# Performance work log

Measured on AMD Instinct MI355X. Metric: run time of the kernel, lower is better.

The kernel has to match this reference:

```python
import jax, jax.numpy as jnp
import numpy as np

N_NODES = 100000
N_EDGES = 800000
NUM_GRAPHS = 64


def _lin_init(key, fan_in, fan_out):
    k1, k2 = jax.random.split(key)
    s = 1.0 / np.sqrt(fan_in)
    W = jax.random.uniform(k1, (fan_in, fan_out), jnp.float32, -s, s)
    b = jax.random.uniform(k2, (fan_out,), jnp.float32, -s, s)
    return W, b


def setup_inputs() -> dict:
    key = jax.random.key(0)
    ks = jax.random.split(key, 20)
    inp = {
        'x1': jax.random.normal(ks[0], (N_NODES, 384), jnp.float32),
        'x2': jax.random.normal(ks[1], (N_NODES, 32), jnp.float32),
        'pe': jax.random.normal(ks[2], (N_NODES, 64), jnp.float32),
        'edge_index': jax.random.randint(ks[3], (2, N_EDGES), 0, N_NODES, jnp.int32),
        'batch': jnp.sort(jax.random.randint(ks[4], (N_NODES,), 0, NUM_GRAPHS, jnp.int32)),
    }
    # parameters (fan_in, fan_out) per __init__ dims
    inp['Wc'], inp['bc'] = _lin_init(ks[5], 384, 192)     # embed_contraction
    inp['Wmf'], inp['bmf'] = _lin_init(ks[6], 192, 256)   # mpnn_feature
    inp['Wgf'], inp['bgf'] = _lin_init(ks[7], 256, 192)   # gcn_feature
    inp['Wmc'], inp['bmc'] = _lin_init(ks[8], 32, 64)     # mpnn_class
    inp['Wgc'], inp['bgc'] = _lin_init(ks[9], 64, 192)    # gcn_class
    inp['Wa1'], inp['ba1'] = _lin_init(ks[10], 192, 256)  # attention_nn[0]
    inp['Wa2'], inp['ba2'] = _lin_init(ks[11], 256, 192)  # attention_nn[2]
    inp['Wgd'], inp['bgd'] = _lin_init(ks[12], 192, 192)  # gcn_decoder
    inp['Wd1'], inp['bd1'] = _lin_init(ks[13], 192, 192)  # mpnn_decoder1
    inp['Wd2'], inp['bd2'] = _lin_init(ks[14], 192, 192)  # mpnn_decoder2
    inp['Wd3'], inp['bd3'] = _lin_init(ks[15], 192, 384)  # mpnn_decoder3
    return inp


def _mpnn(x, src, dst, W, b):
    # aggr='add': scatter-add gathered source features to targets, then Linear
    agg = jax.ops.segment_sum(x[src], dst, num_segments=N_NODES)
    return agg @ W + b


def _gcn(x, src, dst, W, b):
    # GCNConv with default self-loops and symmetric deg^-1/2 normalization
    h = x @ W
    deg = jax.ops.segment_sum(jnp.ones(src.shape[0], h.dtype), dst, num_segments=N_NODES) + 1.0
    dinv = jax.lax.rsqrt(deg)
    norm = dinv[src] * dinv[dst]
    agg = jax.ops.segment_sum(h[src] * norm[:, None], dst, num_segments=N_NODES)
    agg = agg + h * (dinv * dinv)[:, None]  # self-loop contribution
    return agg + b


def reference(x1, x2, pe, edge_index, batch,
              Wc, bc, Wmf, bmf, Wgf, bgf, Wmc, bmc, Wgc, bgc,
              Wa1, ba1, Wa2, ba2, Wgd, bgd, Wd1, bd1, Wd2, bd2, Wd3, bd3):
    src, dst = edge_index[0], edge_index[1]
    pe3 = jnp.concatenate([pe, pe, pe], axis=-1)  # [N, 192]

    # ---- encoder ----
    x1_res = jax.nn.relu(x1 @ Wc + bc)            # [N, 192]
    h = x1_res + pe3
    h = jax.nn.relu(_mpnn(h, src, dst, Wmf, bmf))  # [N, 256]
    h = jax.nn.relu(_gcn(h, src, dst, Wgf, bgf))   # [N, 192]
    c = jax.nn.relu(_mpnn(x2, src, dst, Wmc, bmc)) # [N, 64]
    c = jax.nn.relu(_gcn(c, src, dst, Wgc, bgc))   # [N, 192]
    z = h + c + x1_res

    # attentional aggregation: gate = attention_nn(z), segment softmax, weighted sum
    gate = jax.nn.relu(z @ Wa1 + ba1) @ Wa2 + ba2   # [N, 192]
    gmax = jax.ops.segment_max(gate, batch, num_segments=NUM_GRAPHS)
    e = jnp.exp(gate - gmax[batch])
    esum = jax.ops.segment_sum(e, batch, num_segments=NUM_GRAPHS)
    alpha = e / esum[batch]
    zg = jax.ops.segment_sum(alpha * z, batch, num_segments=NUM_GRAPHS)  # [B, 192]

    # ---- decoder ----
    z1 = zg[batch]                                  # broadcast graph embedding to nodes
    z1_res = jax.nn.relu(_gcn(z1, src, dst, Wgd, bgd))
    t = z1_res + pe3
    t = jax.nn.relu(_mpnn(t, src, dst, Wd1, bd1))
    t = jax.nn.relu(_mpnn(t, src, dst, Wd2, bd2)) + z1_res
    out = jax.nn.relu(_mpnn(t, src, dst, Wd3, bd3))  # [N, 384]
    return out
```

## Files before the change

kernel.cpp:

```cpp
#include <hip/hip_runtime.h>
#include <math.h>

#define N_NODES 100000
#define N_EDGES 800000
#define NGRAPH  64

typedef __attribute__((ext_vector_type(8))) __bf16 bf16x8;
typedef __attribute__((ext_vector_type(4))) float f32x4;

static __device__ __forceinline__ unsigned flip_f(float x) {
  unsigned u = __float_as_uint(x);
  return u ^ ((u & 0x80000000u) ? 0xFFFFFFFFu : 0x80000000u);
}
static __device__ __forceinline__ float unflip_f(unsigned m) {
  unsigned u = m ^ ((m & 0x80000000u) ? 0x80000000u : 0xFFFFFFFFu);
  return __uint_as_float(u);
}
static __device__ __forceinline__ unsigned short f2bf(float x) {
  unsigned u = __float_as_uint(x);
  u += 0x7fffu + ((u >> 16) & 1u);
  return (unsigned short)(u >> 16);
}
static __device__ __forceinline__ unsigned pk2(float a, float b) {
  return (unsigned)f2bf(a) | ((unsigned)f2bf(b) << 16);
}
static __device__ __forceinline__ float bf2f(unsigned short h) {
  return __uint_as_float((unsigned)h << 16);
}
static __device__ __forceinline__ void unpack8(uint4 w, float* f) {
  f[0] = __uint_as_float(w.x << 16); f[1] = __uint_as_float(w.x & 0xFFFF0000u);
  f[2] = __uint_as_float(w.y << 16); f[3] = __uint_as_float(w.y & 0xFFFF0000u);
  f[4] = __uint_as_float(w.z << 16); f[5] = __uint_as_float(w.z & 0xFFFF0000u);
  f[6] = __uint_as_float(w.w << 16); f[7] = __uint_as_float(w.w & 0xFFFF0000u);
}
static __device__ __forceinline__ uint4 pack8(const float* f) {
  uint4 w;
  w.x = pk2(f[0], f[1]); w.y = pk2(f[2], f[3]);
  w.z = pk2(f[4], f[5]); w.w = pk2(f[6], f[7]);
  return w;
}

__global__ void hist_k(const int* __restrict__ dst, int* __restrict__ cnt) {
  int e = blockIdx.x * 256 + threadIdx.x;
  if (e < N_EDGES) atomicAdd(&cnt[dst[e]], 1);
}

__global__ void dinv_k(const int* __restrict__ cnt, float* __restrict__ dinv) {
  int i = blockIdx.x * 256 + threadIdx.x;
  if (i < N_NODES) dinv[i] = rsqrtf((float)cnt[i] + 1.0f);
}

__global__ void scan_block_k(const int* __restrict__ cnt, int* __restrict__ rs,
                             int* __restrict__ bsum) {
  __shared__ int s[256];
  int t = threadIdx.x, i = blockIdx.x * 256 + t;
  int v = (i < N_NODES) ? cnt[i] : 0;
  s[t] = v; __syncthreads();
  for (int off = 1; off < 256; off <<= 1) {
    int a = (t >= off) ? s[t - off] : 0;
    __syncthreads();
    s[t] += a;
    __syncthreads();
  }
  if (i < N_NODES) rs[i] = s[t] - v;
  if (t == 255) bsum[blockIdx.x] = s[255];
}

__global__ void scan_bsum_k(int* __restrict__ bsum, int nb) {
  __shared__ int s[512];
  int t = threadIdx.x;
  int v = (t < nb) ? bsum[t] : 0;
  s[t] = v; __syncthreads();
  for (int off = 1; off < 512; off <<= 1) {
    int a = (t >= off) ? s[t - off] : 0;
    __syncthreads();
    s[t] += a;
    __syncthreads();
  }
  if (t < nb) bsum[t] = s[t] - v;
}

__global__ void scan_add_k(int* __restrict__ rs, int* __restrict__ cursor,
                           const int* __restrict__ bsum) {
  int i = blockIdx.x * 256 + threadIdx.x;
  if (i < N_NODES) {
    int r = rs[i] + bsum[i >> 8];
    rs[i] = r;
    cursor[i] = r;
  }
}

__global__ void build_k(const int* __restrict__ src, const int* __restrict__ dst,
                        int* __restrict__ cursor, int* __restrict__ srcs) {
  int e = blockIdx.x * 256 + threadIdx.x;
  if (e < N_EDGES) {
    int d = dst[e];
    int p = atomicAdd(&cursor[d], 1);
    srcs[p] = src[e];
  }
}

__global__ void graph_starts_k(const int* __restrict__ batch, int* __restrict__ gstart) {
  int g = threadIdx.x;
  if (g > NGRAPH) return;
  if (g == NGRAPH) { gstart[NGRAPH] = N_NODES; return; }
  int lo = 0, hi = N_NODES;
  while (lo < hi) {
    int mid = (lo + hi) >> 1;
    if (batch[mid] < g) lo = mid + 1; else hi = mid;
  }
  gstart[g] = lo;
}

template <typename AT, int K, int KT, int NT, bool OUT_F32>
__global__ __launch_bounds__(256, 2)
void gemm_t(const AT* __restrict__ A, const float* __restrict__ B,
            const float* __restrict__ bias,
            const unsigned short* __restrict__ add1,
            const unsigned short* __restrict__ add2,
            void* __restrict__ Cv, int M, int F, int relu,
            const float* __restrict__ pe3src, unsigned short* __restrict__ C2) {
  constexpr int BN = 16 * NT;
  constexpr int KTILES = K / KT;
  constexpr int NSTEP = KT / 32;
  constexpr int KOCTS = KT / 8;
  constexpr int STK = KT + 8;
  __shared__ unsigned short Bs[BN * STK];
  const int tid = threadIdx.x;
  const int wave = tid >> 6, lane = tid & 63;
  const int quad = lane >> 4, l16 = lane & 15;
  const int row0 = blockIdx.x * 64;
  const int col0 = blockIdx.y * BN;
  const int arow = row0 + wave * 16 + l16;
  const bool aok = arow < M;
  const int nsub = tid & 31;
  const int koct = tid >> 5;

  f32x4 acc[NT];
#pragma unroll
  for (int j = 0; j < NT; j++) acc[j] = (f32x4){0.f, 0.f, 0.f, 0.f};

#pragma unroll
  for (int kt = 0; kt < KTILES; ++kt) {
    if (kt) __syncthreads();

    float4 av[sizeof(AT) == 4 ? 2 * NSTEP : 1];
    uint4 ah[sizeof(AT) == 4 ? 1 : NSTEP];
    if constexpr (sizeof(AT) == 4) {
      const float* ap = (const float*)A + (size_t)arow * K + kt * KT + quad * 8;
#pragma unroll
      for (int s = 0; s < NSTEP; s++) {
        av[2 * s] = aok ? *(const float4*)(ap + s * 32) : make_float4(0.f, 0.f, 0.f, 0.f);
        av[2 * s + 1] = aok ? *(const float4*)(ap + s * 32 + 4) : make_float4(0.f, 0.f, 0.f, 0.f);
      }
    } else {
      const unsigned short* ap = (const unsigned short*)A + (size_t)arow * K + kt * KT + quad * 8;
#pragma unroll
      for (int s = 0; s < NSTEP; s++)
        ah[s] = aok ? *(const uint4*)(ap + s * 32) : make_uint4(0, 0, 0, 0);
    }

#pragma unroll
    for (int ob = 0; ob < KOCTS; ob += 8) {
      int oct = ob + koct;
      if (oct < KOCTS) {
#pragma unroll
        for (int nc = 0; nc < BN; nc += 32) {
          int n = nc + nsub;
          const float* bp = B + (size_t)(kt * KT + oct * 8) * F + col0 + n;
          uint4 w;
          w.x = pk2(bp[0], bp[(size_t)1 * F]);
          w.y = pk2(bp[(size_t)2 * F], bp[(size_t)3 * F]);
          w.z = pk2(bp[(size_t)4 * F], bp[(size_t)5 * F]);
          w.w = pk2(bp[(size_t)6 * F], bp[(size_t)7 * F]);
          *(uint4*)&Bs[n * STK + oct * 8] = w;
        }
      }
    }
    __syncthreads();

#pragma unroll
    for (int s = 0; s < NSTEP; ++s) {
      bf16x8 afr;
      if constexpr (sizeof(AT) == 4) {
        uint4 t;
        t.x = pk2(av[2 * s].x, av[2 * s].y);
        t.y = pk2(av[2 * s].z, av[2 * s].w);
        t.z = pk2(av[2 * s + 1].x, av[2 * s + 1].y);
        t.w = pk2(av[2 * s + 1].z, av[2 * s + 1].w);
        afr = *(bf16x8*)&t;
      } else {
        afr = *(bf16x8*)&ah[s];
      }
#pragma unroll
      for (int nt = 0; nt < NT; nt++) {
        bf16x8 bfr = *(const bf16x8*)&Bs[(nt * 16 + l16) * STK + s * 32 + quad * 8];
        acc[nt] = __builtin_amdgcn_mfma_f32_16x16x32_bf16(afr, bfr, acc[nt], 0, 0, 0);
      }
    }
  }

  float* Cf = (float*)Cv;
  unsigned short* Ch = (unsigned short*)Cv;
#pragma unroll
  for (int r = 0; r < 4; r++) {
    int row = row0 + wave * 16 + quad * 4 + r;
    if (row >= M) continue;
#pragma unroll
    for (int nt = 0; nt < NT; nt++) {
      int col = col0 + nt * 16 + l16;
      float v = acc[nt][r];
      if (bias) v += bias[col];
      if (relu) v = fmaxf(v, 0.f);
      size_t off = (size_t)row * F + col;
      if (add1) v += bf2f(add1[off]);
      if (add2) v += bf2f(add2[off]);
      if (OUT_F32) Cf[off] = v; else Ch[off] = f2bf(v);
      if (C2) C2[off] = f2bf(v + pe3src[(size_t)row * 64 + (col & 63)]);
    }
  }
}

__global__ __launch_bounds__(256)
void gemm_kernel(const float* __restrict__ A, const float* __restrict__ B,
                 const float* __restrict__ bias, float* __restrict__ C,
                 int M, int K, int F) {
  __shared__ float Asm[16][65];
  __shared__ float Bsm[16][65];
  const int tid = threadIdx.x;
  const int tx = tid & 15, ty = tid >> 4;
  const int row0 = blockIdx.x * 64;
  const int col0 = blockIdx.y * 64;
  float acc[4][4];
#pragma unroll
  for (int i = 0; i < 4; i++)
#pragma unroll
    for (int j = 0; j < 4; j++) acc[i][j] = 0.f;

  for (int k0 = 0; k0 < K; k0 += 16) {
#pragma unroll
    for (int l = 0; l < 4; l++) {
      int idx = tid + l * 256;
      int m = idx >> 4, k = idx & 15;
      int r = row0 + m;
      Asm[k][m] = (r < M) ? A[(size_t)r * K + k0 + k] : 0.f;
    }
#pragma unroll
    for (int l = 0; l < 4; l++) {
      int idx = tid + l * 256;
      int k = idx >> 6, n = idx & 63;
      Bsm[k][n] = B[(size_t)(k0 + k) * F + col0 + n];
    }
    __syncthreads();
#pragma unroll
    for (int k = 0; k < 16; k++) {
      float a[4], b[4];
#pragma unroll
      for (int i = 0; i < 4; i++) a[i] = Asm[k][ty * 4 + i];
#pragma unroll
      for (int j = 0; j < 4; j++) b[j] = Bsm[k][tx * 4 + j];
#pragma unroll
      for (int i = 0; i < 4; i++)
#pragma unroll
        for (int j = 0; j < 4; j++) acc[i][j] += a[i] * b[j];
    }
    __syncthreads();
  }
#pragma unroll
  for (int i = 0; i < 4; i++) {
    int r = row0 + ty * 4 + i;
    if (r >= M) continue;
#pragma unroll
    for (int j = 0; j < 4; j++) {
      int c = col0 + tx * 4 + j;
      float v = acc[i][j];
      if (bias) v += bias[c];
      C[(size_t)r * F + c] = v;
    }
  }
}

template <int F>
__global__ void agg_mpnn_bf(const unsigned short* __restrict__ x, const int* __restrict__ rowstart,
                            const int* __restrict__ cnt, const int* __restrict__ srcs,
                            unsigned short* __restrict__ out) {
  constexpr int F8 = F / 8;
  int t = blockIdx.x * 256 + threadIdx.x;
  if (t >= N_NODES * F8) return;
  int i = t / F8, c = (t - i * F8) * 8;
  float a[8] = {0.f, 0.f, 0.f, 0.f, 0.f, 0.f, 0.f, 0.f};
  int e = rowstart[i], e1 = e + cnt[i];
  for (; e < e1; ++e) {
    int s = srcs[e];
    uint4 w = *(const uint4*)(x + (size_t)s * F + c);
    float f[8]; unpack8(w, f);
#pragma unroll
    for (int j = 0; j < 8; j++) a[j] += f[j];
  }
  *(uint4*)(out + (size_t)i * F + c) = pack8(a);
}

template <int F, bool RELU, bool HAS_BIAS>
__global__ void agg_gcn_bf(const unsigned short* __restrict__ x, const int* __restrict__ rowstart,
                           const int* __restrict__ cnt, const int* __restrict__ srcs,
                           const float* __restrict__ dinv, const float* __restrict__ bias,
                           unsigned short* __restrict__ out) {
  constexpr int F8 = F / 8;
  int t = blockIdx.x * 256 + threadIdx.x;
  if (t >= N_NODES * F8) return;
  int i = t / F8, c = (t - i * F8) * 8;
  float a[8] = {0.f, 0.f, 0.f, 0.f, 0.f, 0.f, 0.f, 0.f};
  int e = rowstart[i], e1 = e + cnt[i];
  for (; e < e1; ++e) {
    int s = srcs[e];
    float w = dinv[s];
    uint4 wv = *(const uint4*)(x + (size_t)s * F + c);
    float f[8]; unpack8(wv, f);
#pragma unroll
    for (int j = 0; j < 8; j++) a[j] += w * f[j];
  }
  float di = dinv[i];
  float sw = di * di;
  uint4 sv = *(const uint4*)(x + (size_t)i * F + c);
  float sf[8]; unpack8(sv, sf);
  float r[8];
#pragma unroll
  for (int j = 0; j < 8; j++) {
    float v = di * a[j] + sw * sf[j];
    if (HAS_BIAS) v += bias[c + j];
    if (RELU) v = fmaxf(v, 0.f);
    r[j] = v;
  }
  *(uint4*)(out + (size_t)i * F + c) = pack8(r);
}

__global__ void agg_x2_k(const float* __restrict__ x, const int* __restrict__ rowstart,
                         const int* __restrict__ cnt, const int* __restrict__ srcs,
                         unsigned short* __restrict__ out) {
  int t = blockIdx.x * 256 + threadIdx.x;
  if (t >= N_NODES * 8) return;
  int i = t >> 3, c = (t & 7) * 4;
  float4 acc = make_float4(0.f, 0.f, 0.f, 0.f);
  int e = rowstart[i], e1 = e + cnt[i];
  for (; e < e1; ++e) {
    int s = srcs[e];
    float4 v = *(const float4*)(x + (size_t)s * 32 + c);
    acc.x += v.x; acc.y += v.y; acc.z += v.z; acc.w += v.w;
  }
  ushort4 o;
  o.x = f2bf(acc.x); o.y = f2bf(acc.y); o.z = f2bf(acc.z); o.w = f2bf(acc.w);
  *(ushort4*)(out + (size_t)i * 32 + c) = o;
}

__global__ void agg_gcn_dec_bf(const float* __restrict__ zgW, const int* __restrict__ rowstart,
                               const int* __restrict__ cnt, const int* __restrict__ srcs,
                               const int* __restrict__ batch, const float* __restrict__ dinv,
                               const float* __restrict__ bias, unsigned short* __restrict__ out,
                               const float* __restrict__ pe, unsigned short* __restrict__ out2) {
  int t = blockIdx.x * 256 + threadIdx.x;
  if (t >= N_NODES * 24) return;
  int i = t / 24, c = (t - i * 24) * 8;
  float a[8] = {0.f, 0.f, 0.f, 0.f, 0.f, 0.f, 0.f, 0.f};
  int e = rowstart[i], e1 = e + cnt[i];
  for (; e < e1; ++e) {
    int s = srcs[e];
    float w = dinv[s];
    const float* v = zgW + (size_t)batch[s] * 192 + c;
#pragma unroll
    for (int j = 0; j < 8; j++) a[j] += w * v[j];
  }
  float di = dinv[i];
  float sw = di * di;
  const float* sv = zgW + (size_t)batch[i] * 192 + c;
  float r[8];
#pragma unroll
  for (int j = 0; j < 8; j++)
    r[j] = fmaxf(di * a[j] + sw * sv[j] + bias[c + j], 0.f);
  *(uint4*)(out + (size_t)i * 192 + c) = pack8(r);
  const float* p = pe + (size_t)i * 64 + (c & 63);
  float r2[8];
#pragma unroll
  for (int j = 0; j < 8; j++) r2[j] = r[j] + p[j];
  *(uint4*)(out2 + (size_t)i * 192 + c) = pack8(r2);
}

__global__ void init_gmax_k(unsigned* __restrict__ gmaxu) {
  int t = blockIdx.x * 256 + threadIdx.x;
  if (t < NGRAPH * 192) gmaxu[t] = 0x007FFFFFu;
}

__global__ void seg_max_k(const float* __restrict__ gate, const int* __restrict__ gstart,
                          unsigned* __restrict__ gmaxu) {
  int g = blockIdx.x, f = threadIdx.x;
  int lo = gstart[g], hi = gstart[g + 1];
  int len = hi - lo;
  if (len <= 0) return;
  int per = (len + gridDim.y - 1) / gridDim.y;
  int a = lo + blockIdx.y * per;
  int b = min(a + per, hi);
  if (a >= b) return;
  float m = -INFINITY;
  for (int i = a; i < b; i++) m = fmaxf(m, gate[(size_t)i * 192 + f]);
  atomicMax(&gmaxu[g * 192 + f], flip_f(m));
}

__global__ void seg_sum_k(const float* __restrict__ gate, const unsigned short* __restrict__ z,
                          const int* __restrict__ gstart, const unsigned* __restrict__ gmaxu,
                          float* __restrict__ esum, float* __restrict__ znum) {
  int g = blockIdx.x, f = threadIdx.x;
  int lo = gstart[g], hi = gstart[g + 1];
  int len = hi - lo;
  if (len <= 0) return;
  int per = (len + gridDim.y - 1) / gridDim.y;
  int a = lo + blockIdx.y * per;
  int b = min(a + per, hi);
  if (a >= b) return;
  float gm = unflip_f(gmaxu[g * 192 + f]);
  float se = 0.f, sz = 0.f;
  for (int i = a; i < b; i++) {
    float e = expf(gate[(size_t)i * 192 + f] - gm);
    se += e;
    sz += e * bf2f(z[(size_t)i * 192 + f]);
  }
  atomicAdd(&esum[g * 192 + f], se);
  atomicAdd(&znum[g * 192 + f], sz);
}

__global__ void zg_fin_k(const float* __restrict__ znum, const float* __restrict__ esum,
                         float* __restrict__ zg) {
  int t = blockIdx.x * 256 + threadIdx.x;
  if (t >= NGRAPH * 192) return;
  float es = esum[t];
  zg[t] = (es > 0.f) ? znum[t] / es : 0.f;
}

extern "C" void kernel_launch(void* const* d_in, const int* in_sizes, int n_in,
                              void* d_out, int out_size, void* d_ws, size_t ws_size,
                              hipStream_t stream) {
  const float* x1 = (const float*)d_in[0];
  const float* x2 = (const float*)d_in[1];
  const float* pe = (const float*)d_in[2];
  const int* ei = (const int*)d_in[3];
  const int* src = ei;
  const int* dst = ei + N_EDGES;
  const int* batch = (const int*)d_in[4];
  const float* Wc  = (const float*)d_in[5];  const float* bc  = (const float*)d_in[6];
  const float* Wmf = (const float*)d_in[7];  const float* bmf = (const float*)d_in[8];
  const float* Wgf = (const float*)d_in[9];  const float* bgf = (const float*)d_in[10];
  const float* Wmc = (const float*)d_in[11]; const float* bmc = (const float*)d_in[12];
  const float* Wgc = (const float*)d_in[13]; const float* bgc = (const float*)d_in[14];
  const float* Wa1 = (const float*)d_in[15]; const float* ba1 = (const float*)d_in[16];
  const float* Wa2 = (const float*)d_in[17]; const float* ba2 = (const float*)d_in[18];
  const float* Wgd = (const float*)d_in[19]; const float* bgd = (const float*)d_in[20];
  const float* Wd1 = (const float*)d_in[21]; const float* bd1 = (const float*)d_in[22];
  const float* Wd2 = (const float*)d_in[23]; const float* bd2 = (const float*)d_in[24];
  const float* Wd3 = (const float*)d_in[25]; const float* bd3 = (const float*)d_in[26];
  float* out = (float*)d_out;

  char* base = (char*)d_ws;
  size_t woff = 0;
  auto walloc = [&](size_t bytes) -> void* {
    void* p = base + woff;
    woff = (woff + bytes + 255) & ~(size_t)255;
    return p;
  };
  unsigned short* P0h = (unsigned short*)walloc((size_t)N_NODES * 192 * 2);
  unsigned short* P1h = (unsigned short*)walloc((size_t)N_NODES * 256 * 2);
  unsigned short* P2h = (unsigned short*)walloc((size_t)N_NODES * 192 * 2);
  unsigned short* P5a = (unsigned short*)walloc((size_t)N_NODES * 32 * 2);
  unsigned short* P5b = (unsigned short*)walloc((size_t)N_NODES * 64 * 2);
  unsigned short* P5c = (unsigned short*)walloc((size_t)N_NODES * 64 * 2);
  float* Pg   = (float*)walloc((size_t)N_NODES * 192 * 4);
  float* dinv = (float*)walloc((size_t)N_NODES * 4);
  unsigned* gmaxu = (unsigned*)walloc((size_t)NGRAPH * 192 * 4);
  float* esum = (float*)walloc((size_t)NGRAPH * 192 * 4);
  float* znum = (float*)walloc((size_t)NGRAPH * 192 * 4);
  float* zg   = (float*)walloc((size_t)NGRAPH * 192 * 4);
  float* zgW  = (float*)walloc((size_t)NGRAPH * 192 * 4);
  int* cnt      = (int*)walloc((size_t)N_NODES * 4);
  int* rowstart = (int*)walloc((size_t)N_NODES * 4);
  int* cursor   = (int*)walloc((size_t)N_NODES * 4);
  int* srcs     = (int*)walloc((size_t)N_EDGES * 4);
  int* bsum     = (int*)walloc(512 * 4);
  int* gstart   = (int*)walloc(80 * 4);

  unsigned short* P3h = (unsigned short*)d_out;
  unsigned short* P4h = (unsigned short*)((float*)d_out + (size_t)N_NODES * 192);

  const int TB = 256;
  hipMemsetAsync(cnt, 0, N_NODES * sizeof(int), stream);
  hipMemsetAsync(esum, 0, 2 * NGRAPH * 192 * sizeof(float), stream);

  hist_k<<<(N_EDGES + TB - 1) / TB, TB, 0, stream>>>(dst, cnt);
  dinv_k<<<(N_NODES + TB - 1) / TB, TB, 0, stream>>>(cnt, dinv);
  int nb = (N_NODES + 255) / 256;
  scan_block_k<<<nb, 256, 0, stream>>>(cnt, rowstart, bsum);
  scan_bsum_k<<<1, 512, 0, stream>>>(bsum, nb);
  scan_add_k<<<nb, 256, 0, stream>>>(rowstart, cursor, bsum);
  build_k<<<(N_EDGES + TB - 1) / TB, TB, 0, stream>>>(src, dst, cursor, srcs);
  graph_starts_k<<<1, 128, 0, stream>>>(batch, gstart);

  const int mb64 = (N_NODES + 63) / 64;
  const int ew24 = (N_NODES * 24 + TB - 1) / TB;
  const int ew8 = (N_NODES * 8 + TB - 1) / TB;

  gemm_t<float, 384, 128, 12, false><<<mb64, 256, 0, stream>>>(x1, Wc, bc, nullptr, nullptr, P0h, N_NODES, 192, 1, pe, P1h);
  agg_mpnn_bf<192><<<ew24, TB, 0, stream>>>(P1h, rowstart, cnt, srcs, P2h);
  gemm_t<unsigned short, 192, 192, 8, false><<<dim3(mb64, 2), 256, 0, stream>>>(P2h, Wmf, bmf, nullptr, nullptr, P1h, N_NODES, 256, 1, nullptr, nullptr);
  gemm_t<unsigned short, 256, 256, 6, false><<<dim3(mb64, 2), 256, 0, stream>>>(P1h, Wgf, nullptr, nullptr, nullptr, P3h, N_NODES, 192, 0, nullptr, nullptr);
  agg_gcn_bf<192, true, true><<<ew24, TB, 0, stream>>>(P3h, rowstart, cnt, srcs, dinv, bgf, P4h);
  agg_x2_k<<<ew8, TB, 0, stream>>>(x2, rowstart, cnt, srcs, P5a);
  gemm_t<unsigned short, 32, 32, 4, false><<<mb64, 256, 0, stream>>>(P5a, Wmc, bmc, nullptr, nullptr, P5b, N_NODES, 64, 1, nullptr, nullptr);
  agg_gcn_bf<64, false, false><<<ew8, TB, 0, stream>>>(P5b, rowstart, cnt, srcs, dinv, nullptr, P5c);
  gemm_t<unsigned short, 64, 64, 6, false><<<dim3(mb64, 2), 256, 0, stream>>>(P5c, Wgc, bgc, P4h, P0h, P0h, N_NODES, 192, 1, nullptr, nullptr);

  gemm_t<unsigned short, 192, 192, 8, false><<<dim3(mb64, 2), 256, 0, stream>>>(P0h, Wa1, ba1, nullptr, nullptr, P1h, N_NODES, 256, 1, nullptr, nullptr);
  gemm_t<unsigned short, 256, 256, 6, true><<<dim3(mb64, 2), 256, 0, stream>>>(P1h, Wa2, ba2, nullptr, nullptr, Pg, N_NODES, 192, 0, nullptr, nullptr);
  init_gmax_k<<<(NGRAPH * 192 + TB - 1) / TB, TB, 0, stream>>>(gmaxu);
  dim3 sg(NGRAPH, 16);
  seg_max_k<<<sg, 192, 0, stream>>>(Pg, gstart, gmaxu);
  seg_sum_k<<<sg, 192, 0, stream>>>(Pg, P0h, gstart, gmaxu, esum, znum);
  zg_fin_k<<<(NGRAPH * 192 + TB - 1) / TB, TB, 0, stream>>>(znum, esum, zg);
  gemm_kernel<<<dim3(1, 3), 256, 0, stream>>>(zg, Wgd, nullptr, zgW, NGRAPH, 192, 192);

  agg_gcn_dec_bf<<<ew24, TB, 0, stream>>>(zgW, rowstart, cnt, srcs, batch, dinv, bgd, P4h, pe, P2h);
  agg_mpnn_bf<192><<<ew24, TB, 0, stream>>>(P2h, rowstart, cnt, srcs, P3h);
  gemm_t<unsigned short, 192, 192, 6, false><<<dim3(mb64, 2), 256, 0, stream>>>(P3h, Wd1, bd1, nullptr, nullptr, P1h, N_NODES, 192, 1, nullptr, nullptr);
  agg_mpnn_bf<192><<<ew24, TB, 0, stream>>>(P1h, rowstart, cnt, srcs, P2h);
  gemm_t<unsigned short, 192, 192, 6, false><<<dim3(mb64, 2), 256, 0, stream>>>(P2h, Wd2, bd2, P4h, nullptr, P3h, N_NODES, 192, 1, nullptr, nullptr);
  agg_mpnn_bf<192><<<ew24, TB, 0, stream>>>(P3h, rowstart, cnt, srcs, P2h);
  gemm_t<unsigned short, 192, 192, 8, true><<<dim3(mb64, 3), 256, 0, stream>>>(P2h, Wd3, bd3, nullptr, nullptr, out, N_NODES, 384, 1, nullptr, nullptr);
  (void)in_sizes; (void)n_in; (void)out_size; (void)ws_size;
}
```

Before: 1.498 ms.

## Pre-convert weights to transposed bf16 once and shrink GEMM K-tiles for occupancy

Adds a single batched kernel that converts all ten weight matrices to bf16 in an [F][K] transposed layout at the start of each call. Each GEMM block then loads its B tile with contiguous 16-byte reads instead of eight strided fp32 loads plus packing per element, which it previously repeated in every one of the roughly 1,500 row blocks. K-tiles are halved and launch bounds raised to allow more resident blocks, which saves LDS and registers but adds more K-loop iterations and barriers. The cost is one extra small launch and about 0.9 MB of workspace.

```diff
diff --git a/kernel.cpp b/kernel.cpp
--- a/kernel.cpp
+++ b/kernel.cpp
@@ -38,6 +38,29 @@
   w.x = pk2(f[0], f[1]); w.y = pk2(f[2], f[3]);
   w.z = pk2(f[4], f[5]); w.w = pk2(f[6], f[7]);
   return w;
+}
+
+struct WJobs {
+  const float* src[10];
+  int K[10];
+  int F[10];
+  int eoff[10];
+  int bend[10];
+};
+
+__global__ void wconv_k(WJobs jb, unsigned short* __restrict__ dst) {
+  int b = blockIdx.x;
+  int j = 0;
+#pragma unroll
+  for (int t = 0; t < 10; t++)
+    if (b >= jb.bend[t]) j = t + 1;
+  int bstart = j ? jb.bend[j - 1] : 0;
+  int local = (b - bstart) * 256 + threadIdx.x;
+  int K = jb.K[j], F = jb.F[j];
+  if (local >= K * F) return;
+  int n = local / K;
+  int k = local - n * K;
+  dst[jb.eoff[j] + local] = f2bf(jb.src[j][(size_t)k * F + n]);
 }
 
 __global__ void hist_k(const int* __restrict__ dst, int* __restrict__ cnt) {
@@ -112,9 +135,9 @@
   gstart[g] = lo;
 }
 
-template <typename AT, int K, int KT, int NT, bool OUT_F32>
-__global__ __launch_bounds__(256, 2)
-void gemm_t(const AT* __restrict__ A, const float* __restrict__ B,
+template <typename AT, int K, int KT, int NT, bool OUT_F32, int OCC>
+__global__ __launch_bounds__(256, OCC)
+void gemm_t(const AT* __restrict__ A, const unsigned short* __restrict__ Bt,
             const float* __restrict__ bias,
             const unsigned short* __restrict__ add1,
             const unsigned short* __restrict__ add2,
@@ -123,7 +146,7 @@
   constexpr int BN = 16 * NT;
   constexpr int KTILES = K / KT;
   constexpr int NSTEP = KT / 32;
-  constexpr int KOCTS = KT / 8;
+  constexpr int KC = KT / 8;
   constexpr int STK = KT + 8;
   __shared__ unsigned short Bs[BN * STK];
   const int tid = threadIdx.x;
@@ -133,8 +156,6 @@
   const int col0 = blockIdx.y * BN;
   const int arow = row0 + wave * 16 + l16;
   const bool aok = arow < M;
-  const int nsub = tid & 31;
-  const int koct = tid >> 5;
 
   f32x4 acc[NT];
 #pragma unroll
@@ -161,21 +182,11 @@
     }
 
 #pragma unroll
-    for (int ob = 0; ob < KOCTS; ob += 8) {
-      int oct = ob + koct;
-      if (oct < KOCTS) {
-#pragma unroll
-        for (int nc = 0; nc < BN; nc += 32) {
-          int n = nc + nsub;
-          const float* bp = B + (size_t)(kt * KT + oct * 8) * F + col0 + n;
-          uint4 w;
-          w.x = pk2(bp[0], bp[(size_t)1 * F]);
-          w.y = pk2(bp[(size_t)2 * F], bp[(size_t)3 * F]);
-          w.z = pk2(bp[(size_t)4 * F], bp[(size_t)5 * F]);
-          w.w = pk2(bp[(size_t)6 * F], bp[(size_t)7 * F]);
-          *(uint4*)&Bs[n * STK + oct * 8] = w;
-        }
-      }
+    for (int idx = tid; idx < BN * KC; idx += 256) {
+      int n = idx / KC;
+      int c = idx - n * KC;
+      uint4 w = *(const uint4*)(Bt + (size_t)(col0 + n) * K + kt * KT + c * 8);
+      *(uint4*)&Bs[n * STK + c * 8] = w;
     }
     __syncthreads();
 
@@ -472,6 +483,7 @@
   unsigned short* P5c = (unsigned short*)walloc((size_t)N_NODES * 64 * 2);
   float* Pg   = (float*)walloc((size_t)N_NODES * 192 * 4);
   float* dinv = (float*)walloc((size_t)N_NODES * 4);
+  unsigned short* Wt = (unsigned short*)walloc((size_t)432128 * 2);
   unsigned* gmaxu = (unsigned*)walloc((size_t)NGRAPH * 192 * 4);
   float* esum = (float*)walloc((size_t)NGRAPH * 192 * 4);
   float* znum = (float*)walloc((size_t)NGRAPH * 192 * 4);
@@ -487,9 +499,33 @@
   unsigned short* P3h = (unsigned short*)d_out;
   unsigned short* P4h = (unsigned short*)((float*)d_out + (size_t)N_NODES * 192);
 
+  const unsigned short* WtWc  = Wt + 0;
+  const unsigned short* WtWmf = Wt + 73728;
+  const unsigned short* WtWgf = Wt + 122880;
+  const unsigned short* WtWmc = Wt + 172032;
+  const unsigned short* WtWgc = Wt + 174080;
+  const unsigned short* WtWa1 = Wt + 186368;
+  const unsigned short* WtWa2 = Wt + 235520;
+  const unsigned short* WtWd1 = Wt + 284672;
+  const unsigned short* WtWd2 = Wt + 321536;
+  const unsigned short* WtWd3 = Wt + 358400;
+
   const int TB = 256;
   hipMemsetAsync(cnt, 0, N_NODES * sizeof(int), stream);
   hipMemsetAsync(esum, 0, 2 * NGRAPH * 192 * sizeof(float), stream);
+
+  WJobs jb;
+  jb.src[0] = Wc;  jb.K[0] = 384; jb.F[0] = 192; jb.eoff[0] = 0;      jb.bend[0] = 288;
+  jb.src[1] = Wmf; jb.K[1] = 192; jb.F[1] = 256; jb.eoff[1] = 73728;  jb.bend[1] = 480;
+  jb.src[2] = Wgf; jb.K[2] = 256; jb.F[2] = 192; jb.eoff[2] = 122880; jb.bend[2] = 672;
+  jb.src[3] = Wmc; jb.K[3] = 32;  jb.F[3] = 64;  jb.eoff[3] = 172032; jb.bend[3] = 680;
+  jb.src[4] = Wgc; jb.K[4] = 64;  jb.F[4] = 192; jb.eoff[4] = 174080; jb.bend[4] = 728;
+  jb.src[5] = Wa1; jb.K[5] = 192; jb.F[5] = 256; jb.eoff[5] = 186368; jb.bend[5] = 920;
+  jb.src[6] = Wa2; jb.K[6] = 256; jb.F[6] = 192; jb.eoff[6] = 235520; jb.bend[6] = 1112;
+  jb.src[7] = Wd1; jb.K[7] = 192; jb.F[7] = 192; jb.eoff[7] = 284672; jb.bend[7] = 1256;
+  jb.src[8] = Wd2; jb.K[8] = 192; jb.F[8] = 192; jb.eoff[8] = 321536; jb.bend[8] = 1400;
+  jb.src[9] = Wd3; jb.K[9] = 192; jb.F[9] = 384; jb.eoff[9] = 358400; jb.bend[9] = 1688;
+  wconv_k<<<1688, 256, 0, stream>>>(jb, Wt);
 
   hist_k<<<(N_EDGES + TB - 1) / TB, TB, 0, stream>>>(dst, cnt);
   dinv_k<<<(N_NODES + TB - 1) / TB, TB, 0, stream>>>(cnt, dinv);
@@ -504,18 +540,18 @@
   const int ew24 = (N_NODES * 24 + TB - 1) / TB;
   const int ew8 = (N_NODES * 8 + TB - 1) / TB;
 
-  gemm_t<float, 384, 128, 12, false><<<mb64, 256, 0, stream>>>(x1, Wc, bc, nullptr, nullptr, P0h, N_NODES, 192, 1, pe, P1h);
+  gemm_t<float, 384, 96, 12, false, 4><<<mb64, 256, 0, stream>>>(x1, WtWc, bc, nullptr, nullptr, P0h, N_NODES, 192, 1, pe, P1h);
   agg_mpnn_bf<192><<<ew24, TB, 0, stream>>>(P1h, rowstart, cnt, srcs, P2h);
-  gemm_t<unsigned short, 192, 192, 8, false><<<dim3(mb64, 2), 256, 0, stream>>>(P2h, Wmf, bmf, nullptr, nullptr, P1h, N_NODES, 256, 1, nullptr, nullptr);
-  gemm_t<unsigned short, 256, 256, 6, false><<<dim3(mb64, 2), 256, 0, stream>>>(P1h, Wgf, nullptr, nullptr, nullptr, P3h, N_NODES, 192, 0, nullptr, nullptr);
+  gemm_t<unsigned short, 192, 96, 8, false, 6><<<dim3(mb64, 2), 256, 0, stream>>>(P2h, WtWmf, bmf, nullptr, nullptr, P1h, N_NODES, 256, 1, nullptr, nullptr);
+  gemm_t<unsigned short, 256, 128, 6, false, 6><<<dim3(mb64, 2), 256, 0, stream>>>(P1h, WtWgf, nullptr, nullptr, nullptr, P3h, N_NODES, 192, 0, nullptr, nullptr);
   agg_gcn_bf<192, true, true><<<ew24, TB, 0, stream>>>(P3h, rowstart, cnt, srcs, dinv, bgf, P4h);
   agg_x2_k<<<ew8, TB, 0, stream>>>(x2, rowstart, cnt, srcs, P5a);
-  gemm_t<unsigned short, 32, 32, 4, false><<<mb64, 256, 0, stream>>>(P5a, Wmc, bmc, nullptr, nullptr, P5b, N_NODES, 64, 1, nullptr, nullptr);
+  gemm_t<unsigned short, 32, 32, 4, false, 6><<<mb64, 256, 0, stream>>>(P5a, WtWmc, bmc, nullptr, nullptr, P5b, N_NODES, 64, 1, nullptr, nullptr);
   agg_gcn_bf<64, false, false><<<ew8, TB, 0, stream>>>(P5b, rowstart, cnt, srcs, dinv, nullptr, P5c);
-  gemm_t<unsigned short, 64, 64, 6, false><<<dim3(mb64, 2), 256, 0, stream>>>(P5c, Wgc, bgc, P4h, P0h, P0h, N_NODES, 192, 1, nullptr, nullptr);
-
-  gemm_t<unsigned short, 192, 192, 8, false><<<dim3(mb64, 2), 256, 0, stream>>>(P0h, Wa1, ba1, nullptr, nullptr, P1h, N_NODES, 256, 1, nullptr, nullptr);
-  gemm_t<unsigned short, 256, 256, 6, true><<<dim3(mb64, 2), 256, 0, stream>>>(P1h, Wa2, ba2, nullptr, nullptr, Pg, N_NODES, 192, 0, nullptr, nullptr);
+  gemm_t<unsigned short, 64, 64, 6, false, 6><<<dim3(mb64, 2), 256, 0, stream>>>(P5c, WtWgc, bgc, P4h, P0h, P0h, N_NODES, 192, 1, nullptr, nullptr);
+
+  gemm_t<unsigned short, 192, 96, 8, false, 6><<<dim3(mb64, 2), 256, 0, stream>>>(P0h, WtWa1, ba1, nullptr, nullptr, P1h, N_NODES, 256, 1, nullptr, nullptr);
+  gemm_t<unsigned short, 256, 128, 6, true, 6><<<dim3(mb64, 2), 256, 0, stream>>>(P1h, WtWa2, ba2, nullptr, nullptr, Pg, N_NODES, 192, 0, nullptr, nullptr);
   init_gmax_k<<<(NGRAPH * 192 + TB - 1) / TB, TB, 0, stream>>>(gmaxu);
   dim3 sg(NGRAPH, 16);
   seg_max_k<<<sg, 192, 0, stream>>>(Pg, gstart, gmaxu);
@@ -525,10 +561,10 @@
 
   agg_gcn_dec_bf<<<ew24, TB, 0, stream>>>(zgW, rowstart, cnt, srcs, batch, dinv, bgd, P4h, pe, P2h);
   agg_mpnn_bf<192><<<ew24, TB, 0, stream>>>(P2h, rowstart, cnt, srcs, P3h);
-  gemm_t<unsigned short, 192, 192, 6, false><<<dim3(mb64, 2), 256, 0, stream>>>(P3h, Wd1, bd1, nullptr, nullptr, P1h, N_NODES, 192, 1, nullptr, nullptr);
+  gemm_t<unsigned short, 192, 96, 6, false, 6><<<dim3(mb64, 2), 256, 0, stream>>>(P3h, WtWd1, bd1, nullptr, nullptr, P1h, N_NODES, 192, 1, nullptr, nullptr);
   agg_mpnn_bf<192><<<ew24, TB, 0, stream>>>(P1h, rowstart, cnt, srcs, P2h);
-  gemm_t<unsigned short, 192, 192, 6, false><<<dim3(mb64, 2), 256, 0, stream>>>(P2h, Wd2, bd2, P4h, nullptr, P3h, N_NODES, 192, 1, nullptr, nullptr);
+  gemm_t<unsigned short, 192, 96, 6, false, 6><<<dim3(mb64, 2), 256, 0, stream>>>(P2h, WtWd2, bd2, P4h, nullptr, P3h, N_NODES, 192, 1, nullptr, nullptr);
   agg_mpnn_bf<192><<<ew24, TB, 0, stream>>>(P3h, rowstart, cnt, srcs, P2h);
-  gemm_t<unsigned short, 192, 192, 8, true><<<dim3(mb64, 3), 256, 0, stream>>>(P2h, Wd3, bd3, nullptr, nullptr, out, N_NODES, 384, 1, nullptr, nullptr);
+  gemm_t<unsigned short, 192, 96, 8, true, 6><<<dim3(mb64, 3), 256, 0, stream>>>(P2h, WtWd3, bd3, nullptr, nullptr, out, N_NODES, 384, 1, nullptr, nullptr);
   (void)in_sizes; (void)n_in; (void)out_size; (void)ws_size;
 }
```

After: 1.426 ms. -4.8%, faster.
